# Kernel tuning notes

Measured on AMD Instinct MI355X. Metric: run time of the kernel, lower is better.

The kernel has to match this reference:

```python
import jax, jax.numpy as jnp
import numpy as np

DEPTH = 2
DIM = 256
MLP = 1024
B = 2
N = 2048


def setup_inputs() -> dict:
    key = jax.random.key(0)
    ks = jax.random.split(key, 6)
    s = 0.02
    d = DIM
    f32 = jnp.float32
    return {
        "x": jax.random.normal(ks[0], (B, N, d), f32),
        "ln1_g": jnp.ones((DEPTH, d), f32),
        "ln1_b": jnp.zeros((DEPTH, d), f32),
        "Wqkv": (jax.random.normal(ks[1], (DEPTH, d, 3 * d), f32) * s),
        "bqkv": jnp.zeros((DEPTH, 3 * d), f32),
        "Wo": (jax.random.normal(ks[2], (DEPTH, d, d), f32) * s),
        "bo": jnp.zeros((DEPTH, d), f32),
        "ln2_g": jnp.ones((DEPTH, d), f32),
        "ln2_b": jnp.zeros((DEPTH, d), f32),
        "W1": (jax.random.normal(ks[3], (DEPTH, d, MLP), f32) * s),
        "b1": jnp.zeros((DEPTH, MLP), f32),
        "W2": (jax.random.normal(ks[4], (DEPTH, MLP, d), f32) * s),
        "b2": jnp.zeros((DEPTH, d), f32),
        "heads": 8,
    }


def _ln(x, g, b, eps=1e-5):
    m = x.mean(-1, keepdims=True)
    v = ((x - m) ** 2).mean(-1, keepdims=True)
    return (x - m) * jax.lax.rsqrt(v + eps) * g + b


def reference(x, ln1_g, ln1_b, Wqkv, bqkv, Wo, bo, ln2_g, ln2_b, W1, b1, W2, b2, heads):
    b, n, dim = x.shape
    hd = dim // heads
    scale = hd ** -0.5
    depth = Wqkv.shape[0]
    out = x
    # NOTE: faithful to original: `x` is never updated inside the loop,
    # so only the last layer's output is returned.
    for i in range(depth):
        y = _ln(x, ln1_g[i], ln1_b[i])
        qkv = y @ Wqkv[i] + bqkv[i]                      # [b,n,3*dim]
        qkv = qkv.reshape(b, n, 3, heads, hd)
        q, k, v = jnp.moveaxis(qkv, 2, 0)                # each [b,n,h,hd]
        q = q.transpose(0, 2, 1, 3)                      # [b,h,n,hd]
        k = k.transpose(0, 2, 1, 3)
        v = v.transpose(0, 2, 1, 3)
        dots = jnp.einsum('bhid,bhjd->bhij', q, k) * scale
        attn = jax.nn.softmax(dots, axis=-1)
        o = jnp.einsum('bhij,bhjd->bhid', attn, v)       # [b,h,n,hd]
        o = o.transpose(0, 2, 1, 3).reshape(b, n, dim)
        o = o @ Wo[i] + bo[i]
        a = o + x                                        # attn residual
        z = _ln(a, ln2_g[i], ln2_b[i])
        m = jax.nn.gelu(z @ W1[i] + b1[i], approximate=False) @ W2[i] + b2[i]
        out = m + a                                      # mlp residual
    return out
```

## Files before the change

kernel.cpp:

```cpp
#include <hip/hip_runtime.h>
#include <hip/hip_bf16.h>
#include <math.h>

#define DEPTHC 2
#define DIMD   256
#define MLPD   1024
#define BB     2
#define NN     2048
#define HH     8
#define HD     32
#define ROWS   (BB * NN)
#define KSPLIT 4

typedef __attribute__((ext_vector_type(8))) short bf16x8;
typedef __attribute__((ext_vector_type(4))) float f32x4;

__device__ __forceinline__ short f2bf(float x) {
    union { float f; unsigned u; } c; c.f = x;
    unsigned u = c.u + (0x7fffu + ((c.u >> 16) & 1u));
    return (short)(u >> 16);
}
__device__ __forceinline__ float bf2f(short s) {
    union { unsigned u; float f; } c; c.u = ((unsigned)(unsigned short)s) << 16;
    return c.f;
}

__global__ __launch_bounds__(256) void transpose_frag(
    const float* __restrict__ Wqkv, const float* __restrict__ Wo,
    const float* __restrict__ W1,   const float* __restrict__ W2,
    short* __restrict__ WqkvF, short* __restrict__ WoF,
    short* __restrict__ W1F,   short* __restrict__ W2F)
{
    __shared__ short Ts[128][72];
    int blk = blockIdx.x;
    const float* W; short* WF; int K, N;
    if (blk < 24)      {           W = Wqkv; WF = WqkvF; K = 256;  N = 768;  }
    else if (blk < 32) { blk -= 24; W = Wo;   WF = WoF;   K = 256;  N = 256;  }
    else if (blk < 64) { blk -= 32; W = W1;   WF = W1F;   K = 256;  N = 1024; }
    else               { blk -= 64; W = W2;   WF = W2F;   K = 1024; N = 256;  }
    const int nkc = K >> 7;
    const int bx  = blk / nkc;
    const int kc  = blk % nkc;
    const int n0  = bx * 64;
    const int k0  = kc * 128;

    const int nc  = threadIdx.x & 63;
    const int kr0 = threadIdx.x >> 6;
#pragma unroll
    for (int i = 0; i < 32; ++i) {
        const int kr = kr0 + i * 4;
        Ts[kr][nc] = f2bf(W[(size_t)(k0 + kr) * N + n0 + nc]);
    }
    __syncthreads();

    short* out = WF + ((size_t)bx * nkc + kc) * 8192;
#pragma unroll
    for (int i = 0; i < 4; ++i) {
        const int u    = threadIdx.x + i * 256;
        const int l16  = u & 15;
        const int quad = (u >> 4) & 3;
        const int nt   = (u >> 6) & 3;
        const int ks   = (u >> 8) & 3;
        const int n    = nt * 16 + l16;
        const int kk   = (ks * 4 + quad) * 8;
        bf16x8 v;
#pragma unroll
        for (int j = 0; j < 8; ++j) v[j] = Ts[kk + j][n];
        *(bf16x8*)&out[(size_t)u * 8] = v;
    }
}

template <int K, bool GELU, bool RES, bool OBF>
__global__ __launch_bounds__(64) void gemm_1w(
    const short* __restrict__ A,
    const short* __restrict__ WF,
    const float* __restrict__ bias, const float* __restrict__ R,
    void* __restrict__ Cv, int N)
{
    __shared__ short Bs[8192];

    const int lane = threadIdx.x;
    const int quad = lane >> 4;
    const int l16  = lane & 15;
    const int n0   = blockIdx.x * 64;
    const int m0   = blockIdx.y * 64;
    constexpr int NKC = K / 128;

    const short* wfb  = WF + (size_t)blockIdx.x * NKC * 8192;
    const short* arow = A + (size_t)(m0 + l16) * K + quad * 8;

    f32x4 acc[4][4] = {};

    bf16x8 af[4], afn[4];
#pragma unroll
    for (int mt = 0; mt < 4; ++mt)
        af[mt] = *(const bf16x8*)(arow + (size_t)mt * 16 * K);

#pragma unroll 1
    for (int kc = 0; kc < NKC; ++kc) {
        const short* src = wfb + (size_t)kc * 8192;
#pragma unroll
        for (int r = 0; r < 16; ++r) {
            const int u = r * 64 + lane;
            *(bf16x8*)&Bs[u * 8] = *(const bf16x8*)&src[(size_t)u * 8];
        }

#pragma unroll
        for (int ks = 0; ks < 4; ++ks) {
            const int knext = kc * 128 + (ks + 1) * 32;
            if (knext < K) {
#pragma unroll
                for (int mt = 0; mt < 4; ++mt)
                    afn[mt] = *(const bf16x8*)(arow + (size_t)mt * 16 * K + knext);
            }
#pragma unroll
            for (int nt = 0; nt < 4; ++nt) {
                const bf16x8 bf = *(const bf16x8*)
                    &Bs[((((ks * 4 + nt) * 4 + quad) * 16) + l16) * 8];
#pragma unroll
                for (int mt = 0; mt < 4; ++mt)
                    acc[mt][nt] = __builtin_amdgcn_mfma_f32_16x16x32_bf16(
                        af[mt], bf, acc[mt][nt], 0, 0, 0);
            }
#pragma unroll
            for (int mt = 0; mt < 4; ++mt) af[mt] = afn[mt];
        }
    }

#pragma unroll
    for (int mt = 0; mt < 4; ++mt)
#pragma unroll
    for (int nt = 0; nt < 4; ++nt)
#pragma unroll
    for (int r = 0; r < 4; ++r) {
        const int row = m0 + mt * 16 + quad * 4 + r;
        const int col = n0 + nt * 16 + l16;
        float v = acc[mt][nt][r] + bias[col];
        if (RES)  v += R[(size_t)row * N + col];
        if (GELU) v = 0.5f * v * (1.f + erff(v * 0.70710678118f));
        if (OBF) ((short*)Cv)[(size_t)row * N + col] = f2bf(v);
        else     ((float*)Cv)[(size_t)row * N + col] = v;
    }
}

__global__ __launch_bounds__(256) void ln_kernel(
    const float* __restrict__ x, const float* __restrict__ g,
    const float* __restrict__ bta, short* __restrict__ y)
{
    const int wave = threadIdx.x >> 6;
    const int lane = threadIdx.x & 63;
    const int row  = blockIdx.x * 4 + wave;
    const int c    = lane * 4;

    const float4 v = *(const float4*)&x[(size_t)row * DIMD + c];
    float s  = v.x + v.y + v.z + v.w;
    float sq = v.x * v.x + v.y * v.y + v.z * v.z + v.w * v.w;
#pragma unroll
    for (int off = 32; off > 0; off >>= 1) {
        s  += __shfl_down(s,  off, 64);
        sq += __shfl_down(sq, off, 64);
    }
    s  = __shfl(s,  0, 64);
    sq = __shfl(sq, 0, 64);

    const float mean = s * (1.f / DIMD);
    const float var  = sq * (1.f / DIMD) - mean * mean;
    const float rstd = rsqrtf(var + 1e-5f);

    const float4 gg = *(const float4*)&g[c];
    const float4 bb = *(const float4*)&bta[c];
    short4 ov;
    ov.x = f2bf((v.x - mean) * rstd * gg.x + bb.x);
    ov.y = f2bf((v.y - mean) * rstd * gg.y + bb.y);
    ov.z = f2bf((v.z - mean) * rstd * gg.z + bb.z);
    ov.w = f2bf((v.w - mean) * rstd * gg.w + bb.w);
    *(short4*)&y[(size_t)row * DIMD + c] = ov;
}

__global__ __launch_bounds__(256) void transpose_v(
    const short* __restrict__ qkv, short* __restrict__ vtg)
{
    __shared__ short Vs[64][33];
    const int tid = threadIdx.x;
    const int bh  = blockIdx.y;
    const int b   = bh >> 3;
    const int h   = bh & 7;
    const int n0  = blockIdx.x * 64;

    const int kk = tid >> 2;
    const int sd = (tid & 3) * 8;
    const bf16x8 tmp = *(const bf16x8*)(
        qkv + ((size_t)(b * NN + n0 + kk)) * (3 * DIMD) + 2 * DIMD + h * HD + sd);
#pragma unroll
    for (int j = 0; j < 8; ++j) Vs[kk][sd + j] = tmp[j];
    __syncthreads();

    const int d  = tid >> 3;
    const int kc = (tid & 7) * 8;
    bf16x8 v;
#pragma unroll
    for (int j = 0; j < 8; ++j) v[j] = Vs[kc + j][d];
    *(bf16x8*)&vtg[((size_t)(bh * HD + d)) * NN + n0 + kc] = v;
}

__global__ __launch_bounds__(256) void attn_mfma(
    const short* __restrict__ qkv, const short* __restrict__ vtg,
    short* __restrict__ pO, float* __restrict__ pl)
{
    __shared__ short Ks[64][40];
    __shared__ short Vs[32][72];
    __shared__ short Ps[4][16][72];

    const int tid  = threadIdx.x;
    const int w    = tid >> 6;
    const int lane = tid & 63;
    const int quad = lane >> 4;
    const int l16  = lane & 15;
    const int bh   = blockIdx.y;
    const int b    = bh >> 3;
    const int h    = bh & 7;
    const int ks   = blockIdx.z;
    const int q0   = blockIdx.x * 64 + w * 16;

    const float scale = 0.17677669529663689f;
    const float shift = 11.090354888959125f;
    const short* base = qkv + (size_t)b * NN * (3 * DIMD);

    const bf16x8 qfrag =
        *(const bf16x8*)(base + (size_t)(q0 + l16) * (3 * DIMD) + h * HD + quad * 8);

    const int skey = tid >> 2;
    const int sd   = (tid & 3) * 8;
    const int vd   = tid >> 3;
    const int vk   = (tid & 7) * 8;

    const short* kgp = base + (size_t)(ks * (NN / KSPLIT) + skey) * (3 * DIMD)
                       + DIMD + h * HD + sd;
    const short* vgp = vtg + ((size_t)bh * HD + vd) * NN
                       + ks * (NN / KSPLIT) + vk;

    f32x4 oacc0 = {0.f, 0.f, 0.f, 0.f};
    f32x4 oacc1 = {0.f, 0.f, 0.f, 0.f};
    float rowsum[4] = {0.f, 0.f, 0.f, 0.f};

    bf16x8 kreg = *(const bf16x8*)kgp;
    bf16x8 vreg = *(const bf16x8*)vgp;

#pragma unroll 1
    for (int t = 0; t < NN / KSPLIT / 64; ++t) {
        __syncthreads();
        *(bf16x8*)&Ks[skey][sd] = kreg;
        *(bf16x8*)&Vs[vd][vk]   = vreg;
        __syncthreads();

        if (t + 1 < NN / KSPLIT / 64) {
            kreg = *(const bf16x8*)(kgp + (size_t)(t + 1) * 64 * (3 * DIMD));
            vreg = *(const bf16x8*)(vgp + (t + 1) * 64);
        }

        f32x4 s[4];
#pragma unroll
        for (int kt = 0; kt < 4; ++kt) {
            const bf16x8 kf = *(const bf16x8*)&Ks[kt * 16 + l16][quad * 8];
            f32x4 z = {0.f, 0.f, 0.f, 0.f};
            s[kt] = __builtin_amdgcn_mfma_f32_16x16x32_bf16(qfrag, kf, z, 0, 0, 0);
        }

#pragma unroll
        for (int kt = 0; kt < 4; ++kt)
#pragma unroll
            for (int r = 0; r < 4; ++r) {
                const float p = __expf(fmaf(s[kt][r], scale, -shift));
                rowsum[r] += p;
                union { float f; unsigned u; } cv; cv.f = p;
                Ps[w][quad * 4 + r][kt * 16 + l16] = (short)(cv.u >> 16);
            }

#pragma unroll
        for (int c = 0; c < 2; ++c) {
            const bf16x8 pf = *(const bf16x8*)&Ps[w][l16][c * 32 + quad * 8];
            const bf16x8 v0 = *(const bf16x8*)&Vs[l16][c * 32 + quad * 8];
            const bf16x8 v1 = *(const bf16x8*)&Vs[16 + l16][c * 32 + quad * 8];
            oacc0 = __builtin_amdgcn_mfma_f32_16x16x32_bf16(pf, v0, oacc0, 0, 0, 0);
            oacc1 = __builtin_amdgcn_mfma_f32_16x16x32_bf16(pf, v1, oacc1, 0, 0, 0);
        }
    }

#pragma unroll
    for (int off = 1; off <= 8; off <<= 1)
#pragma unroll
        for (int r = 0; r < 4; ++r)
            rowsum[r] += __shfl_xor(rowsum[r], off, 64);

#pragma unroll
    for (int r = 0; r < 4; ++r) {
        const size_t rg = (size_t)bh * NN + q0 + quad * 4 + r;
        pO[(rg * KSPLIT + ks) * HD + l16]      = f2bf(oacc0[r]);
        pO[(rg * KSPLIT + ks) * HD + 16 + l16] = f2bf(oacc1[r]);
        if (l16 == 0) pl[rg * KSPLIT + ks] = rowsum[r];
    }
}

__global__ __launch_bounds__(256) void attn_merge(
    const short* __restrict__ pO, const float* __restrict__ pl,
    short* __restrict__ o)
{
    const int idx = blockIdx.x * 256 + threadIdx.x;
    const int r   = idx >> 5;
    const int d   = idx & 31;

    float L = 0.f, O = 0.f;
#pragma unroll
    for (int s = 0; s < KSPLIT; ++s) {
        L += pl[r * KSPLIT + s];
        O += bf2f(pO[(size_t)(r * KSPLIT + s) * HD + d]);
    }
    const int bh = r >> 11;
    const int q  = r & (NN - 1);
    const int b  = bh >> 3;
    const int h  = bh & 7;
    o[((size_t)(b * NN + q)) * DIMD + h * HD + d] = f2bf(O / L);
}

extern "C" void kernel_launch(void* const* d_in, const int* in_sizes, int n_in,
                              void* d_out, int out_size, void* d_ws, size_t ws_size,
                              hipStream_t stream)
{
    const int L = DEPTHC - 1;
    const float* x     = (const float*)d_in[0];
    const float* ln1_g = (const float*)d_in[1]  + L * DIMD;
    const float* ln1_b = (const float*)d_in[2]  + L * DIMD;
    const float* Wqkv  = (const float*)d_in[3]  + (size_t)L * DIMD * 3 * DIMD;
    const float* bqkv  = (const float*)d_in[4]  + L * 3 * DIMD;
    const float* Wo    = (const float*)d_in[5]  + (size_t)L * DIMD * DIMD;
    const float* bo    = (const float*)d_in[6]  + L * DIMD;
    const float* ln2_g = (const float*)d_in[7]  + L * DIMD;
    const float* ln2_b = (const float*)d_in[8]  + L * DIMD;
    const float* W1    = (const float*)d_in[9]  + (size_t)L * DIMD * MLPD;
    const float* b1    = (const float*)d_in[10] + L * MLPD;
    const float* W2    = (const float*)d_in[11] + (size_t)L * MLPD * DIMD;
    const float* b2    = (const float*)d_in[12] + L * DIMD;
    float* out = (float*)d_out;

    short* WqkvF = (short*)d_ws;
    short* WoF   = WqkvF + 12 * 2 * 8192;
    short* W1F   = WoF   + 4 * 2 * 8192;
    short* W2F   = W1F   + 16 * 2 * 8192;
    short* ybf   = W2F   + 4 * 8 * 8192;
    short* zbf   = ybf   + (size_t)ROWS * DIMD;
    short* qkvbf = zbf   + (size_t)ROWS * DIMD;
    short* vtg   = qkvbf + (size_t)ROWS * 3 * DIMD;
    short* obf   = vtg   + (size_t)16 * HD * NN;
    short* pO    = obf   + (size_t)ROWS * DIMD;
    short* m1bf  = pO    + (size_t)16 * NN * KSPLIT * HD;
    float* pl    = (float*)(m1bf + (size_t)ROWS * MLPD);
    float* a     = pl + (size_t)16 * NN * KSPLIT;

    transpose_frag<<<96, 256, 0, stream>>>(Wqkv, Wo, W1, W2, WqkvF, WoF, W1F, W2F);

    ln_kernel<<<ROWS / 4, 256, 0, stream>>>(x, ln1_g, ln1_b, ybf);

    gemm_1w<256, false, false, true><<<dim3(12, 64), 64, 0, stream>>>(
        ybf, WqkvF, bqkv, nullptr, qkvbf, 3 * DIMD);

    transpose_v<<<dim3(NN / 64, BB * HH), 256, 0, stream>>>(qkvbf, vtg);

    attn_mfma<<<dim3(NN / 64, BB * HH, KSPLIT), 256, 0, stream>>>(qkvbf, vtg, pO, pl);
    attn_merge<<<(16 * NN * HD) / 256, 256, 0, stream>>>(pO, pl, obf);

    gemm_1w<256, false, true, false><<<dim3(4, 64), 64, 0, stream>>>(
        obf, WoF, bo, x, a, DIMD);

    ln_kernel<<<ROWS / 4, 256, 0, stream>>>(a, ln2_g, ln2_b, zbf);

    gemm_1w<256, true, false, true><<<dim3(16, 64), 64, 0, stream>>>(
        zbf, W1F, b1, nullptr, m1bf, MLPD);

    gemm_1w<1024, false, true, false><<<dim3(4, 64), 64, 0, stream>>>(
        m1bf, W2F, b2, a, out, DIMD);
}
```

Baseline: 168.4 us.

## Split GEMM K dimension across four waves with shared-memory reduction

Replaces the single-wave 64x64 GEMM tile with a 256-thread block in which each of four waves handles a quarter of the K dimension, staging its own weight fragments in private LDS. Partial accumulators are then reduced through shared memory in two passes before the bias, residual and GELU epilogue. The aim is more waves per tile and more latency hiding, which matters for the small-grid Wo and W2 GEMMs. The cost is extra LDS traffic and barriers for the reduction, and the register prefetch of the A operand is dropped.

```diff
diff --git a/kernel.cpp b/kernel.cpp
--- a/kernel.cpp
+++ b/kernel.cpp
@@ -71,75 +71,93 @@
 }
 
 template <int K, bool GELU, bool RES, bool OBF>
-__global__ __launch_bounds__(64) void gemm_1w(
+__global__ __launch_bounds__(256) void gemm_ks(
     const short* __restrict__ A,
     const short* __restrict__ WF,
     const float* __restrict__ bias, const float* __restrict__ R,
     void* __restrict__ Cv, int N)
 {
-    __shared__ short Bs[8192];
-
-    const int lane = threadIdx.x;
+    __shared__ short smem[4][4096];
+
+    const int tid  = threadIdx.x;
+    const int w    = tid >> 6;
+    const int lane = tid & 63;
     const int quad = lane >> 4;
     const int l16  = lane & 15;
     const int n0   = blockIdx.x * 64;
     const int m0   = blockIdx.y * 64;
-    constexpr int NKC = K / 128;
+    constexpr int NKC   = K / 128;
+    constexpr int SLICE = K / 4;
+    constexpr int NHC   = SLICE / 64;
 
     const short* wfb  = WF + (size_t)blockIdx.x * NKC * 8192;
     const short* arow = A + (size_t)(m0 + l16) * K + quad * 8;
+    short* reg = smem[w];
 
     f32x4 acc[4][4] = {};
 
-    bf16x8 af[4], afn[4];
-#pragma unroll
-    for (int mt = 0; mt < 4; ++mt)
-        af[mt] = *(const bf16x8*)(arow + (size_t)mt * 16 * K);
-
-#pragma unroll 1
-    for (int kc = 0; kc < NKC; ++kc) {
-        const short* src = wfb + (size_t)kc * 8192;
-#pragma unroll
-        for (int r = 0; r < 16; ++r) {
-            const int u = r * 64 + lane;
-            *(bf16x8*)&Bs[u * 8] = *(const bf16x8*)&src[(size_t)u * 8];
-        }
-
-#pragma unroll
-        for (int ks = 0; ks < 4; ++ks) {
-            const int knext = kc * 128 + (ks + 1) * 32;
-            if (knext < K) {
-#pragma unroll
-                for (int mt = 0; mt < 4; ++mt)
-                    afn[mt] = *(const bf16x8*)(arow + (size_t)mt * 16 * K + knext);
-            }
+#pragma unroll
+    for (int hc = 0; hc < NHC; ++hc) {
+        const int kbase = w * SLICE + hc * 64;
+        const short* src = wfb +
+            ((size_t)(kbase >> 7) * 1024 + (size_t)((kbase >> 6) & 1) * 512) * 8;
+#pragma unroll
+        for (int i = 0; i < 8; ++i)
+            *(bf16x8*)&reg[(i * 64 + lane) * 8] =
+                *(const bf16x8*)&src[(size_t)(i * 64 + lane) * 8];
+
+#pragma unroll
+        for (int ksl = 0; ksl < 2; ++ksl) {
+            const int kk = kbase + ksl * 32;
+            bf16x8 af[4];
+#pragma unroll
+            for (int mt = 0; mt < 4; ++mt)
+                af[mt] = *(const bf16x8*)(arow + (size_t)mt * 16 * K + kk);
 #pragma unroll
             for (int nt = 0; nt < 4; ++nt) {
                 const bf16x8 bf = *(const bf16x8*)
-                    &Bs[((((ks * 4 + nt) * 4 + quad) * 16) + l16) * 8];
+                    &reg[(((ksl * 4 + nt) * 4 + quad) * 16 + l16) * 8];
 #pragma unroll
                 for (int mt = 0; mt < 4; ++mt)
                     acc[mt][nt] = __builtin_amdgcn_mfma_f32_16x16x32_bf16(
                         af[mt], bf, acc[mt][nt], 0, 0, 0);
             }
-#pragma unroll
-            for (int mt = 0; mt < 4; ++mt) af[mt] = afn[mt];
-        }
-    }
-
-#pragma unroll
-    for (int mt = 0; mt < 4; ++mt)
-#pragma unroll
-    for (int nt = 0; nt < 4; ++nt)
-#pragma unroll
-    for (int r = 0; r < 4; ++r) {
-        const int row = m0 + mt * 16 + quad * 4 + r;
-        const int col = n0 + nt * 16 + l16;
-        float v = acc[mt][nt][r] + bias[col];
-        if (RES)  v += R[(size_t)row * N + col];
-        if (GELU) v = 0.5f * v * (1.f + erff(v * 0.70710678118f));
-        if (OBF) ((short*)Cv)[(size_t)row * N + col] = f2bf(v);
-        else     ((float*)Cv)[(size_t)row * N + col] = v;
+        }
+    }
+
+#pragma unroll
+    for (int p = 0; p < 2; ++p) {
+        __syncthreads();
+#pragma unroll
+        for (int mtl = 0; mtl < 2; ++mtl)
+#pragma unroll
+            for (int nt = 0; nt < 4; ++nt)
+                *(f32x4*)&smem[w][((mtl * 4 + nt) * 64 + lane) * 8] = acc[2 * p + mtl][nt];
+        __syncthreads();
+        if ((w >> 1) == p) {
+            const int mtl = w & 1;
+            const int mt  = 2 * p + mtl;
+#pragma unroll
+            for (int nt = 0; nt < 4; ++nt) {
+                const int idx = ((mtl * 4 + nt) * 64 + lane) * 8;
+                const f32x4 s0 = *(const f32x4*)&smem[0][idx];
+                const f32x4 s1 = *(const f32x4*)&smem[1][idx];
+                const f32x4 s2 = *(const f32x4*)&smem[2][idx];
+                const f32x4 s3 = *(const f32x4*)&smem[3][idx];
+                const f32x4 s  = (s0 + s1) + (s2 + s3);
+                const int col  = n0 + nt * 16 + l16;
+                const float bb = bias[col];
+#pragma unroll
+                for (int r = 0; r < 4; ++r) {
+                    const int row = m0 + mt * 16 + quad * 4 + r;
+                    float v = s[r] + bb;
+                    if (RES)  v += R[(size_t)row * N + col];
+                    if (GELU) v = 0.5f * v * (1.f + erff(v * 0.70710678118f));
+                    if (OBF) ((short*)Cv)[(size_t)row * N + col] = f2bf(v);
+                    else     ((float*)Cv)[(size_t)row * N + col] = v;
+                }
+            }
+        }
     }
 }
 
@@ -360,7 +378,7 @@
 
     ln_kernel<<<ROWS / 4, 256, 0, stream>>>(x, ln1_g, ln1_b, ybf);
 
-    gemm_1w<256, false, false, true><<<dim3(12, 64), 64, 0, stream>>>(
+    gemm_ks<256, false, false, true><<<dim3(12, 64), 256, 0, stream>>>(
         ybf, WqkvF, bqkv, nullptr, qkvbf, 3 * DIMD);
 
     transpose_v<<<dim3(NN / 64, BB * HH), 256, 0, stream>>>(qkvbf, vtg);
@@ -368,14 +386,14 @@
     attn_mfma<<<dim3(NN / 64, BB * HH, KSPLIT), 256, 0, stream>>>(qkvbf, vtg, pO, pl);
     attn_merge<<<(16 * NN * HD) / 256, 256, 0, stream>>>(pO, pl, obf);
 
-    gemm_1w<256, false, true, false><<<dim3(4, 64), 64, 0, stream>>>(
+    gemm_ks<256, false, true, false><<<dim3(4, 64), 256, 0, stream>>>(
         obf, WoF, bo, x, a, DIMD);
 
     ln_kernel<<<ROWS / 4, 256, 0, stream>>>(a, ln2_g, ln2_b, zbf);
 
-    gemm_1w<256, true, false, true><<<dim3(16, 64), 64, 0, stream>>>(
+    gemm_ks<256, true, false, true><<<dim3(16, 64), 256, 0, stream>>>(
         zbf, W1F, b1, nullptr, m1bf, MLPD);
 
-    gemm_1w<1024, false, true, false><<<dim3(4, 64), 64, 0, stream>>>(
+    gemm_ks<1024, false, true, false><<<dim3(4, 64), 256, 0, stream>>>(
         m1bf, W2F, b2, a, out, DIMD);
 }
```

Result: no change. 168.9 us (+0.3%).
